# Performance work log

Hardware: AMD Instinct MI355X
Metric: run time of the kernel (lower is better)

The kernel has to match this reference:

```python
import jax, jax.numpy as jnp
import numpy as np

NT, NS, NH = 2000, 512, 64


def setup_inputs() -> dict:
    key = jax.random.key(0)
    ks = jax.random.split(key, 11)
    # forcings: precipitation >=0, temperature ~ N(0,5), PET >=0
    P = jax.random.uniform(ks[0], (NT, NS), dtype=jnp.float32) * 10.0
    T = jax.random.normal(ks[1], (NT, NS), dtype=jnp.float32) * 5.0
    E = jax.random.uniform(ks[2], (NT, NS), dtype=jnp.float32) * 2.0
    # parameters, matching reset_parameters() ranges
    w = jax.random.uniform(ks[3], (NH,), minval=-1.0, maxval=2.0)
    wk1 = jax.random.uniform(ks[4], (NH,), minval=-1.0, maxval=1.0)
    wk2 = jax.random.uniform(ks[5], (NH,), minval=-1.0, maxval=1.0)
    we1 = jax.random.uniform(ks[6], (NH,), minval=-1.0, maxval=1.0)
    we2 = jax.random.uniform(ks[7], (NH,), minval=-1.0, maxval=1.0)
    wl = jax.random.uniform(ks[8], (NH,), minval=-1.0, maxval=1.0)
    wo = jax.random.uniform(ks[9], (NH,), minval=-1.0, maxval=1.0)
    wc = jax.random.uniform(ks[10], (NH,), minval=-1.0, maxval=1.0)
    return {"P": P, "T": T, "E": E, "w": w, "wk1": wk1, "wk2": wk2,
            "we1": we1, "we2": we2, "wl": wl, "wo": wo, "wc": wc}


def _soil_cq_forward(P, T, E, w, wk1, wk2, we1, we2, wl, wo, wc):
    nh = w.shape[0]
    ns = P.shape[1]
    a = jax.nn.softmax(wo)          # dropout is identity in eval mode
    ew = jnp.exp(w) + 1.0           # snow melt factor
    sk1 = jax.nn.sigmoid(wk1)
    sk2 = jax.nn.sigmoid(wk2)
    se1 = jax.nn.sigmoid(we1)
    se2 = jax.nn.sigmoid(we2)
    L = jnp.exp(wl)                 # soil layer capacity
    r = 1.0 / sk2 / (1.0 + jnp.exp(wc))  # residence-time factor for C

    def step(carry, inp):
        s, h1, h2 = carry           # each (ns, nh)
        p, t, e = inp               # each (ns,)
        # --- SnowBucket (nm=0 -> m = min(sm, s) over all columns) ---
        sm = jax.nn.relu(t)[:, None] * ew
        m = jnp.minimum(sm, s)
        s_new = s - m + ((t < 0) * p)[:, None]
        x = ((t > 0) * p)[:, None] + m
        # --- SoilBucket ---
        e1 = e[:, None] * se1
        e2 = e[:, None] * se2
        h1a = jax.nn.relu(h1 + h2 + x - L)
        q1 = h1a * sk1
        h2a = jnp.minimum(h1a + h2 + x, L)
        q2 = h2a * sk2
        q3 = h2a * sk2              # original computes q3 with wk2 as well
        h1n = jax.nn.relu(h1a - q1 - e1)
        h2n = jax.nn.relu(h2a - q2 - e2 - q3)
        # --- outputs ---
        Qs1 = jnp.sum(q1 * a, axis=1)
        Qs2 = jnp.sum(q2 * a, axis=1)
        Qk = Qs1 + Qs2
        c = jnp.mean(q2 * a * r + 1e-5, axis=1) / (Qk + 1e-5)
        qs = jnp.stack([Qs1, Qs2, jnp.zeros_like(Qs1)], axis=-1)  # Qs[:, :, 2] stays 0
        return (s_new, h1n, h2n), (s_new, h1n, h2n, Qk, c, qs)

    z = jnp.zeros((ns, nh), P.dtype)
    _, (S, H1, H2, Q, C, Qs) = jax.lax.scan(step, (z, z, z), (P, T, E))
    return (Q, C, S, H1, H2, Qs)


def reference(P, T, E, w, wk1, wk2, we1, we2, wl, wo, wc):
    return _soil_cq_forward(P, T, E, w, wk1, wk2, we1, we2, wl, wo, wc)
```

## Files before the change

kernel.cpp:

```cpp
#include <hip/hip_runtime.h>


constexpr int NT = 2000;
constexpr int NS = 512;
constexpr int NH = 64;
constexpr int CHUNK = 50;

__device__ __forceinline__ float readlane_f(float v, int k) {
    return __int_as_float(__builtin_amdgcn_readlane(__float_as_int(v), k));
}

template<int CTRL>
__device__ __forceinline__ float dpp_add(float v) {
    int sh = __builtin_amdgcn_update_dpp(0, __float_as_int(v), CTRL, 0xf, 0xf, true);
    return v + __int_as_float(sh);
}

__global__ void __launch_bounds__(64, 1)
soil_cq_kernel(const float* __restrict__ P, const float* __restrict__ T,
               const float* __restrict__ E,
               const float* __restrict__ w,  const float* __restrict__ wk1,
               const float* __restrict__ wk2, const float* __restrict__ we1,
               const float* __restrict__ we2, const float* __restrict__ wl,
               const float* __restrict__ wo,  const float* __restrict__ wc,
               float* __restrict__ out)
{
    const int site = blockIdx.x;
    const int lane = threadIdx.x;

    float wo_l = wo[lane];
    float mx = wo_l;
    #pragma unroll
    for (int off = 32; off; off >>= 1) mx = fmaxf(mx, __shfl_xor(mx, off));
    float ex = expf(wo_l - mx);
    float ssum = ex;
    #pragma unroll
    for (int off = 32; off; off >>= 1) ssum += __shfl_xor(ssum, off);
    const float a   = ex / ssum;
    const float ew  = expf(w[lane]) + 1.0f;
    const float sk1 = 1.0f / (1.0f + expf(-wk1[lane]));
    const float sk2 = 1.0f / (1.0f + expf(-wk2[lane]));
    const float se1 = 1.0f / (1.0f + expf(-we1[lane]));
    const float se2 = 1.0f / (1.0f + expf(-we2[lane]));
    const float L   = expf(wl[lane]);
    const float r   = 1.0f / sk2 / (1.0f + expf(wc[lane]));
    const float ar  = a * r;

    float* Qo  = out;
    float* Co  = out + (size_t)NT * NS;
    float* So  = out + (size_t)2 * NT * NS;
    float* H1o = So  + (size_t)NT * NS * NH;
    float* H2o = H1o + (size_t)NT * NS * NH;
    float* Qso = H2o + (size_t)NT * NS * NH;

    float* optr = nullptr;
    int    ostride = 0;
    if      (lane == 0) { optr = Qo  + site;                 ostride = NS;     }
    else if (lane == 1) { optr = Co  + site;                 ostride = NS;     }
    else if (lane == 2) { optr = Qso + (size_t)site * 3;     ostride = NS * 3; }
    else if (lane == 3) { optr = Qso + (size_t)site * 3 + 1; ostride = NS * 3; }
    else if (lane == 4) { optr = Qso + (size_t)site * 3 + 2; ostride = NS * 3; }

    float s = 0.f, h1 = 0.f, h2 = 0.f;
    size_t sidx = (size_t)site * NH + lane;

    float pv = 0.f, tv = 0.f, evv = 0.f;
    if (lane < CHUNK) {
        const size_t fb = (size_t)lane * NS + site;
        pv = P[fb]; tv = T[fb]; evv = E[fb];
    }

    for (int cb = 0; cb < NT / CHUNK; ++cb) {
        float pn = 0.f, tn = 0.f, en = 0.f;
        if (cb + 1 < NT / CHUNK && lane < CHUNK) {
            const size_t fb = ((size_t)(cb + 1) * CHUNK + lane) * NS + site;
            pn = P[fb]; tn = T[fb]; en = E[fb];
        }

        #pragma unroll 5
        for (int k = 0; k < CHUNK; ++k) {
            const float p = readlane_f(pv, k);
            const float t = readlane_f(tv, k);
            const float e = readlane_f(evv, k);

            const float tpos  = fmaxf(t, 0.f);
            const float psnow = (t < 0.f) ? p : 0.f;
            const float prain = (t > 0.f) ? p : 0.f;

            const float smv  = tpos * ew;
            const float m    = fminf(smv, s);
            const float snew = s - m + psnow;
            const float x    = prain + m;
            const float hh   = h1 + h2 + x;
            const float h1a  = fmaxf(hh - L, 0.f);
            const float q1   = h1a * sk1;
            const float h2a  = fminf(h1a + h2 + x, L);
            const float q2   = h2a * sk2;
            const float e1   = e * se1;
            const float e2   = e * se2;
            const float h1n  = fmaxf(h1a - q1 - e1, 0.f);
            const float h2n  = fmaxf(h2a - q2 - e2 - q2, 0.f);

            So[sidx]  = snew;
            H1o[sidx] = h1n;
            H2o[sidx] = h2n;

            float v1 = q1 * a;
            float v2 = q2 * a;
            float v3 = q2 * ar;
            v1 = dpp_add<0x111>(v1); v2 = dpp_add<0x111>(v2); v3 = dpp_add<0x111>(v3);
            v1 = dpp_add<0x112>(v1); v2 = dpp_add<0x112>(v2); v3 = dpp_add<0x112>(v3);
            v1 = dpp_add<0x114>(v1); v2 = dpp_add<0x114>(v2); v3 = dpp_add<0x114>(v3);
            v1 = dpp_add<0x118>(v1); v2 = dpp_add<0x118>(v2); v3 = dpp_add<0x118>(v3);
            v1 = dpp_add<0x142>(v1); v2 = dpp_add<0x142>(v2); v3 = dpp_add<0x142>(v3);
            v1 = dpp_add<0x143>(v1); v2 = dpp_add<0x143>(v2); v3 = dpp_add<0x143>(v3);

            const float t1 = readlane_f(v1, 63);
            const float t2 = readlane_f(v2, 63);
            const float t3 = readlane_f(v3, 63);
            const float Qk = t1 + t2;
            const float c  = (t3 * (1.0f / NH) + 1e-5f) / (Qk + 1e-5f);

            if (lane < 5) {
                float oval = (lane == 0) ? Qk
                           : (lane == 1) ? c
                           : (lane == 2) ? t1
                           : (lane == 3) ? t2
                           : 0.f;
                *optr = oval;
                optr += ostride;
            }

            s = snew; h1 = h1n; h2 = h2n;
            sidx += (size_t)NS * NH;
        }

        pv = pn; tv = tn; evv = en;
    }
}

extern "C" void kernel_launch(void* const* d_in, const int* in_sizes, int n_in,
                              void* d_out, int out_size, void* d_ws, size_t ws_size,
                              hipStream_t stream) {
    const float* P   = (const float*)d_in[0];
    const float* T   = (const float*)d_in[1];
    const float* E   = (const float*)d_in[2];
    const float* w   = (const float*)d_in[3];
    const float* wk1 = (const float*)d_in[4];
    const float* wk2 = (const float*)d_in[5];
    const float* we1 = (const float*)d_in[6];
    const float* we2 = (const float*)d_in[7];
    const float* wl  = (const float*)d_in[8];
    const float* wo  = (const float*)d_in[9];
    const float* wc  = (const float*)d_in[10];

    soil_cq_kernel<<<NS, 64, 0, stream>>>(P, T, E, w, wk1, wk2, we1, we2, wl,
                                          wo, wc, (float*)d_out);
}
```

Baseline: 1.153 ms.

## Split time scan into checkpoint pass and parallel segment replay

```diff
diff --git a/kernel.cpp b/kernel.cpp
--- a/kernel.cpp
+++ b/kernel.cpp
@@ -4,7 +4,10 @@
 constexpr int NT = 2000;
 constexpr int NS = 512;
 constexpr int NH = 64;
-constexpr int CHUNK = 50;
+constexpr int K    = 125;
+constexpr int NGRP = 16;
+constexpr int CH1  = 50;
+constexpr int CH2  = 25;
 
 __device__ __forceinline__ float readlane_f(float v, int k) {
     return __int_as_float(__builtin_amdgcn_readlane(__float_as_int(v), k));
@@ -17,16 +20,100 @@
 }
 
 __global__ void __launch_bounds__(64, 1)
-soil_cq_kernel(const float* __restrict__ P, const float* __restrict__ T,
-               const float* __restrict__ E,
-               const float* __restrict__ w,  const float* __restrict__ wk1,
-               const float* __restrict__ wk2, const float* __restrict__ we1,
-               const float* __restrict__ we2, const float* __restrict__ wl,
-               const float* __restrict__ wo,  const float* __restrict__ wc,
-               float* __restrict__ out)
+soil_phase1(const float* __restrict__ P, const float* __restrict__ T,
+            const float* __restrict__ E,
+            const float* __restrict__ w,  const float* __restrict__ wk1,
+            const float* __restrict__ wk2, const float* __restrict__ we1,
+            const float* __restrict__ we2, const float* __restrict__ wl,
+            float* __restrict__ out)
 {
     const int site = blockIdx.x;
     const int lane = threadIdx.x;
+
+    const float ew  = expf(w[lane]) + 1.0f;
+    const float sk1 = 1.0f / (1.0f + expf(-wk1[lane]));
+    const float sk2 = 1.0f / (1.0f + expf(-wk2[lane]));
+    const float se1 = 1.0f / (1.0f + expf(-we1[lane]));
+    const float se2 = 1.0f / (1.0f + expf(-we2[lane]));
+    const float L   = expf(wl[lane]);
+
+    float* So  = out + (size_t)2 * NT * NS;
+    float* H1o = So  + (size_t)NT * NS * NH;
+    float* H2o = H1o + (size_t)NT * NS * NH;
+
+    float s = 0.f, h1 = 0.f, h2 = 0.f;
+    const size_t base = (size_t)site * NH + lane;
+    const size_t STEP = (size_t)NS * NH;
+
+    float pv = 0.f, tv = 0.f, evv = 0.f;
+    if (lane < CH1) {
+        const size_t fb = (size_t)lane * NS + site;
+        pv = P[fb]; tv = T[fb]; evv = E[fb];
+    }
+
+    int nextCk = K - 1;
+
+    for (int cb = 0; cb < NT / CH1; ++cb) {
+        float pn = 0.f, tn = 0.f, en = 0.f;
+        if (cb + 1 < NT / CH1 && lane < CH1) {
+            const size_t fb = ((size_t)(cb + 1) * CH1 + lane) * NS + site;
+            pn = P[fb]; tn = T[fb]; en = E[fb];
+        }
+
+        #pragma unroll 5
+        for (int k = 0; k < CH1; ++k) {
+            const int t = cb * CH1 + k;
+            const float p = readlane_f(pv, k);
+            const float tt = readlane_f(tv, k);
+            const float e = readlane_f(evv, k);
+
+            const float tpos  = fmaxf(tt, 0.f);
+            const float psnow = (tt < 0.f) ? p : 0.f;
+            const float prain = (tt > 0.f) ? p : 0.f;
+            const float smv  = tpos * ew;
+            const float m    = fminf(smv, s);
+            const float snew = s - m + psnow;
+            const float x    = prain + m;
+            const float hh   = h1 + h2 + x;
+            const float h1a  = fmaxf(hh - L, 0.f);
+            const float q1   = h1a * sk1;
+            const float h2a  = fminf(h1a + h2 + x, L);
+            const float q2   = h2a * sk2;
+            const float e1   = e * se1;
+            const float e2   = e * se2;
+            const float h1n  = fmaxf(h1a - q1 - e1, 0.f);
+            const float h2n  = fmaxf(h2a - q2 - e2 - q2, 0.f);
+
+            if (t == nextCk) {
+                const size_t ix = (size_t)t * STEP + base;
+                So[ix]  = snew;
+                H1o[ix] = h1n;
+                H2o[ix] = h2n;
+                nextCk += K;
+            }
+
+            s = snew; h1 = h1n; h2 = h2n;
+        }
+        pv = pn; tv = tn; evv = en;
+    }
+}
+
+__global__ void __launch_bounds__(256, 8)
+soil_phase2(const float* __restrict__ P, const float* __restrict__ T,
+            const float* __restrict__ E,
+            const float* __restrict__ w,  const float* __restrict__ wk1,
+            const float* __restrict__ wk2, const float* __restrict__ we1,
+            const float* __restrict__ we2, const float* __restrict__ wl,
+            const float* __restrict__ wo,  const float* __restrict__ wc,
+            float* __restrict__ out)
+{
+    const int tid  = threadIdx.x;
+    const int wid  = tid >> 6;
+    const int lane = tid & 63;
+    const int gx   = blockIdx.x;
+    const int site = gx & (NS - 1);
+    const int grp  = (gx >> 9) * 4 + wid;
+    const int t0   = grp * K;
 
     float wo_l = wo[lane];
     float mx = wo_l;
@@ -60,25 +147,35 @@
     else if (lane == 2) { optr = Qso + (size_t)site * 3;     ostride = NS * 3; }
     else if (lane == 3) { optr = Qso + (size_t)site * 3 + 1; ostride = NS * 3; }
     else if (lane == 4) { optr = Qso + (size_t)site * 3 + 2; ostride = NS * 3; }
+    if (optr) optr += (size_t)t0 * ostride;
+
+    const size_t STEP = (size_t)NS * NH;
+    const size_t base = (size_t)site * NH + lane;
+    size_t sidx = (size_t)t0 * STEP + base;
 
     float s = 0.f, h1 = 0.f, h2 = 0.f;
-    size_t sidx = (size_t)site * NH + lane;
+    if (grp != 0) {
+        const size_t cx = (size_t)(t0 - 1) * STEP + base;
+        s  = So[cx];
+        h1 = H1o[cx];
+        h2 = H2o[cx];
+    }
 
     float pv = 0.f, tv = 0.f, evv = 0.f;
-    if (lane < CHUNK) {
-        const size_t fb = (size_t)lane * NS + site;
+    if (lane < CH2) {
+        const size_t fb = ((size_t)t0 + lane) * NS + site;
         pv = P[fb]; tv = T[fb]; evv = E[fb];
     }
 
-    for (int cb = 0; cb < NT / CHUNK; ++cb) {
+    for (int cb = 0; cb < K / CH2; ++cb) {
         float pn = 0.f, tn = 0.f, en = 0.f;
-        if (cb + 1 < NT / CHUNK && lane < CHUNK) {
-            const size_t fb = ((size_t)(cb + 1) * CHUNK + lane) * NS + site;
+        if (cb + 1 < K / CH2 && lane < CH2) {
+            const size_t fb = ((size_t)t0 + (size_t)(cb + 1) * CH2 + lane) * NS + site;
             pn = P[fb]; tn = T[fb]; en = E[fb];
         }
 
         #pragma unroll 5
-        for (int k = 0; k < CHUNK; ++k) {
+        for (int k = 0; k < CH2; ++k) {
             const float p = readlane_f(pv, k);
             const float t = readlane_f(tv, k);
             const float e = readlane_f(evv, k);
@@ -86,7 +183,6 @@
             const float tpos  = fmaxf(t, 0.f);
             const float psnow = (t < 0.f) ? p : 0.f;
             const float prain = (t > 0.f) ? p : 0.f;
-
             const float smv  = tpos * ew;
             const float m    = fminf(smv, s);
             const float snew = s - m + psnow;
@@ -132,9 +228,8 @@
             }
 
             s = snew; h1 = h1n; h2 = h2n;
-            sidx += (size_t)NS * NH;
-        }
-
+            sidx += STEP;
+        }
         pv = pn; tv = tn; evv = en;
     }
 }
@@ -154,6 +249,9 @@
     const float* wo  = (const float*)d_in[9];
     const float* wc  = (const float*)d_in[10];
 
-    soil_cq_kernel<<<NS, 64, 0, stream>>>(P, T, E, w, wk1, wk2, we1, we2, wl,
-                                          wo, wc, (float*)d_out);
-}
+    soil_phase1<<<NS, 64, 0, stream>>>(P, T, E, w, wk1, wk2, we1, we2, wl,
+                                       (float*)d_out);
+    soil_phase2<<<NS * NGRP / 4, 256, 0, stream>>>(P, T, E, w, wk1, wk2, we1,
+                                                   we2, wl, wo, wc,
+                                                   (float*)d_out);
+}
```

Result: faster. 1.020 ms (-11.5%).
